# Kernel optimization log

Measured on AMD Instinct MI355X. Metric: run time of the kernel, lower is better.

## Reference

```python
import jax, jax.numpy as jnp
import numpy as np

K = 8          # opt.pk, explicit precision cutoff
MARGIN = 0.2   # opt.margin
NEG = -1e30    # sentinel for masked sort keys


def setup_inputs() -> dict:
    key = jax.random.key(0)
    k1, k2 = jax.random.split(key)
    batch_reprs = jax.random.normal(k1, (4096, 512), dtype=jnp.float32)
    batch_labels = jax.random.randint(k2, (4096,), 0, 64)
    return {"batch_reprs": batch_reprs, "batch_labels": batch_labels}


def _forward(batch_reprs, batch_labels):
    B = batch_reprs.shape[0]
    dt = batch_reprs.dtype
    # cls_match_mat: 1 if same class
    match = (batch_labels[:, None] == batch_labels[None, :]).astype(dt)
    # pairwise euclidean distance (squared=False), safe sqrt at zero diagonal
    sq = jnp.sum(batch_reprs * batch_reprs, axis=1)
    res = jnp.maximum(sq[:, None] - 2.0 * (batch_reprs @ batch_reprs.T) + sq[None, :], 0.0)
    zero = res <= 0.0
    d = jnp.where(zero, 0.0, jnp.sqrt(jnp.where(zero, 1.0, res)))
    sim_hat = -d + (1.0 - match) * MARGIN  # use_margin=True path
    # rank via double argsort (descending similarity -> rank 1 = best)
    order = jnp.argsort(-sim_hat, axis=1)
    rank = jnp.argsort(order, axis=1).astype(dt) + 1.0
    pos_nums = jnp.sum(match, axis=1)
    ks = jnp.minimum(pos_nums, jnp.asarray(K + 1, dt))[:, None]  # k_mat per row
    w = 1.0 / jnp.log2(rank + 1.0) + 1.0  # DCG-style rank weight
    # false positives: not same class, within top-k_i
    fp_mask = (match < 1.0) & (rank <= ks)
    fp_nums = jnp.sum(fp_mask, axis=1)  # |N| per row
    # false negatives: same class, beyond top-k_i
    fn_mask = (match > 0.0) & (rank > ks)
    fp_term = jnp.sum(jnp.where(fp_mask, sim_hat * w, 0.0))
    # per-row variable-size topk over false negatives, vectorized:
    # mask non-FN entries to -inf, sort desc, keep first fp_nums[i] entries
    fn_key = jnp.where(fn_mask, sim_hat, NEG)
    fn_order = jnp.argsort(-fn_key, axis=1)
    sorted_sim = jnp.take_along_axis(sim_hat, fn_order, axis=1)
    sorted_w = jnp.take_along_axis(w, fn_order, axis=1)
    sorted_valid = jnp.take_along_axis(fn_mask, fn_order, axis=1)
    take = (jnp.arange(B)[None, :].astype(dt) < fp_nums[:, None]) & sorted_valid
    fn_term = jnp.sum(jnp.where(take, sorted_sim * sorted_w, 0.0))
    # rows with fp_num==0 contribute 0 to both terms, matching the host loop
    return fp_term - fn_term


def reference(batch_reprs, batch_labels):
    return _forward(batch_reprs, batch_labels)
```

## Files before the change

kernel.cpp:

```cpp
#include <hip/hip_runtime.h>
#include <math.h>

#define BB 4096
#define DD 512
#define KTOP 9
#define MARGIN_F 0.2f

typedef __attribute__((ext_vector_type(8))) short short8;
typedef __attribute__((ext_vector_type(4))) float f32x4;
typedef unsigned long long u64;

__device__ unsigned short g_Rhi[(size_t)BB * DD];
__device__ u64 g_cmask[64 * 64];

__device__ __forceinline__ unsigned short f2bf(float x) {
  unsigned u = __float_as_uint(x);
  u += 0x7fffu + ((u >> 16) & 1u);
  return (unsigned short)(u >> 16);
}

__device__ __forceinline__ void gload16(void* lds, const void* g) {
  __builtin_amdgcn_global_load_lds(
      (const __attribute__((address_space(1))) void*)g,
      (__attribute__((address_space(3))) void*)lds, 16, 0, 0);
}

__device__ __forceinline__ float ord16val(unsigned o16) {
  unsigned e = (o16 << 16) | 0x8000u;
  unsigned s = (e & 0x80000000u) ? (e ^ 0x80000000u) : ~e;
  return __uint_as_float(s);
}

__device__ __forceinline__ unsigned wavemax32_dpp(unsigned c) {
#define MSTEP(CTRL, RM)                                                        \
  {                                                                            \
    unsigned o = (unsigned)__builtin_amdgcn_update_dpp(0, (int)c, CTRL, RM, 0xf, false); \
    if (o > c) c = o;                                                          \
  }
  MSTEP(0xB1, 0xf) MSTEP(0x4E, 0xf) MSTEP(0x141, 0xf) MSTEP(0x140, 0xf)
  MSTEP(0x142, 0xa) MSTEP(0x143, 0xc)
#undef MSTEP
  return (unsigned)__builtin_amdgcn_readlane((int)c, 63);
}

__device__ __forceinline__ int wavesum_dpp(int c) {
#define SSTEP(CTRL, RM)                                                        \
  c += __builtin_amdgcn_update_dpp(0, c, CTRL, RM, 0xf, false);
  SSTEP(0xB1, 0xf) SSTEP(0x4E, 0xf) SSTEP(0x141, 0xf) SSTEP(0x140, 0xf)
  SSTEP(0x142, 0xa) SSTEP(0x143, 0xc)
#undef SSTEP
  return __builtin_amdgcn_readlane(c, 63);
}

__device__ __forceinline__ unsigned u4c(const uint4& f, int q) {
  return q == 0 ? f.x : q == 1 ? f.y : q == 2 ? f.z : f.w;
}

__global__ __launch_bounds__(64) void splitsq(const float* __restrict__ R,
                                              float* __restrict__ sq) {
  const int row = blockIdx.x, lane = threadIdx.x;
  const float4* r4 = (const float4*)(R + (size_t)row * DD);
  float4 a = r4[lane], b = r4[lane + 64];
  float xs[8] = {a.x, a.y, a.z, a.w, b.x, b.y, b.z, b.w};
  unsigned short hs[8];
  float s = 0.f;
  #pragma unroll
  for (int q = 0; q < 8; ++q) {
    float x = xs[q];
    s += x * x;
    hs[q] = f2bf(x);
  }
  const size_t base = (size_t)row * DD;
  *(ushort4*)&g_Rhi[base + lane * 4]       = *(ushort4*)&hs[0];
  *(ushort4*)&g_Rhi[base + 256 + lane * 4] = *(ushort4*)&hs[4];
  #pragma unroll
  for (int off = 32; off; off >>= 1) s += __shfl_down(s, off);
  if (lane == 0) sq[row] = s;
}

__global__ __launch_bounds__(64) void buildmask(const int* __restrict__ labels) {
  __shared__ int slab[BB];
  const int c = blockIdx.x, lane = threadIdx.x;
  for (int i = lane; i < BB / 4; i += 64) ((int4*)slab)[i] = ((const int4*)labels)[i];
  __syncthreads();
  u64 m = 0;
  #pragma unroll
  for (int e = 0; e < 64; ++e) {
    int j = 512 * (e >> 3) + 8 * lane + (e & 7);
    m |= (u64)(slab[j] == c) << e;
  }
  g_cmask[c * 64 + lane] = m;
}

__global__ __launch_bounds__(256) void simgemm_sq(const int* __restrict__ labels,
                                                  const float* __restrict__ sq,
                                                  unsigned short* __restrict__ simq) {
  const int x = blockIdx.x & 7;
  const int c = blockIdx.x >> 3;
  const int bj = 4 * x + (c >> 5);
  const int bi = c & 31;
  const int i0 = bi * 128, j0 = bj * 128;

  __shared__ __align__(16) unsigned char smembytes[35840];
  unsigned short (*kbuf)[2][4096] = (unsigned short (*)[2][4096])smembytes;

  const int tid = threadIdx.x;
  const int wid = tid >> 6, lane = tid & 63;
  const int wr = wid >> 1, wc = wid & 1;
  const int lrow = lane & 15, kblk = lane >> 4;

  f32x4 acc[4][4] = {};

  auto stage = [&](int buf, int k0) {
    const int sr = lane & 15;
    const int sc = (lane >> 4) * 8;
    #pragma unroll
    for (int i = 0; i < 2; ++i) {
      const int chunk = 2 * wid + i;
      const int r = chunk * 16 + sr;
      gload16(&kbuf[buf][0][chunk * 512], &g_Rhi[(size_t)(i0 + r) * DD + k0 + sc]);
      gload16(&kbuf[buf][1][chunk * 512], &g_Rhi[(size_t)(j0 + r) * DD + k0 + sc]);
    }
  };

  stage(0, 0);

  for (int step = 0; step < 16; ++step) {
    const int cur = step & 1;
    __syncthreads();
    if (step < 15) stage(cur ^ 1, (step + 1) * 32);

    short8 a[4], b[4];
    #pragma unroll
    for (int m = 0; m < 4; ++m)
      a[m] = *(const short8*)&kbuf[cur][0][(wr * 4 + m) * 512 + lane * 8];
    #pragma unroll
    for (int n = 0; n < 4; ++n)
      b[n] = *(const short8*)&kbuf[cur][1][(wc * 4 + n) * 512 + lane * 8];

    #pragma unroll
    for (int m = 0; m < 4; ++m) {
      #pragma unroll
      for (int n = 0; n < 4; ++n) {
        acc[m][n] = __builtin_amdgcn_mfma_f32_16x16x32_bf16(a[m], b[n], acc[m][n], 0, 0, 0);
      }
    }
  }

  __syncthreads();
  unsigned short (*T)[132] = (unsigned short (*)[132])smembytes;
  float* sqi = (float*)(smembytes + 33792);
  float* sqj = (float*)(smembytes + 34304);
  int* labi  = (int*)(smembytes + 34816);
  int* labj  = (int*)(smembytes + 35328);
  if (tid < 128) { sqi[tid] = sq[i0 + tid]; labi[tid] = labels[i0 + tid]; }
  else { int t2 = tid - 128; sqj[t2] = sq[j0 + t2]; labj[t2] = labels[j0 + t2]; }
  __syncthreads();

  #pragma unroll
  for (int m = 0; m < 4; ++m) {
    const int rbase = wr * 64 + m * 16 + kblk * 4;
    #pragma unroll
    for (int n = 0; n < 4; ++n) {
      const int ccol = wc * 64 + n * 16 + lrow;
      const float sqc = sqj[ccol];
      const int lc_ = labj[ccol];
      #pragma unroll
      for (int reg = 0; reg < 4; ++reg) {
        const int r = rbase + reg;
        float res = sqi[r] - 2.0f * acc[m][n][reg] + sqc;
        float dd = (res <= 0.f) ? 0.f : sqrtf(res);
        float sv = -dd + ((labi[r] != lc_) ? MARGIN_F : 0.f);
        unsigned su = __float_as_uint(sv);
        unsigned ord = su ^ ((unsigned)((int)su >> 31) | 0x80000000u);
        T[r][ccol] = (unsigned short)(ord >> 16);
      }
    }
  }
  __syncthreads();

  const int srow0 = tid >> 4, scol0 = (tid & 15) * 8;
  #pragma unroll
  for (int p = 0; p < 8; ++p) {
    const int r = p * 16 + srow0;
    short8 w = *(const short8*)&T[r][scol0];
    *(short8*)&simq[(size_t)(i0 + r) * BB + j0 + scol0] = w;
  }
}

#define EKEY(e) ((((u4c(v[(e) >> 3], ((e) & 7) >> 1) >> (16 * ((e) & 1))) & 0xffffu) << 13) \
                 | (lbase - (unsigned)((512 * ((e) >> 3) + ((e) & 7)) << 1)                 \
                    + (unsigned)((mask >> (e)) & 1ull)))

#define TOP2UPD(k, a, b) {                                                     \
  unsigned _mx = ((k) > (a)) ? (k) : (a);                                      \
  unsigned _mn = ((k) > (a)) ? (a) : (k);                                      \
  (a) = _mx;                                                                   \
  (b) = (_mn > (b)) ? _mn : (b); }

__global__ __launch_bounds__(256) void rowproc6(const unsigned short* __restrict__ simq,
                                                const int* __restrict__ labels,
                                                float* __restrict__ partials) {
  const int tid = threadIdx.x;
  const int lane = tid & 63;
  const int row = blockIdx.x * 4 + (tid >> 6);

  const uint4* rowp = (const uint4*)(simq + (size_t)row * BB);
  uint4 v[8];
  #pragma unroll
  for (int s = 0; s < 8; ++s) v[s] = rowp[lane + s * 64];

  const int myl = labels[row];
  const u64 mask = g_cmask[myl * 64 + lane];
  const unsigned lbase = (unsigned)((4095 - 8 * lane) << 1);

  unsigned h1 = 0, h2 = 0;
  #pragma unroll
  for (int e = 0; e < 64; ++e) {
    unsigned k = EKEY(e);
    TOP2UPD(k, h1, h2);
  }
  const int pos = wavesum_dpp(__popcll(mask));
  const int ks = min(pos, KTOP);

  unsigned kth = 0;
  float fp = 0.f; int fpn = 0;
  #pragma unroll
  for (int t = 0; t < KTOP; ++t) {
    if (t < ks) {
      unsigned g = wavemax32_dpp(h1);
      if (!(g & 1u)) { fp += ord16val(g >> 13) * (1.f / log2f((float)(t + 2)) + 1.f); fpn++; }
      if (t == ks - 1) kth = g;
      if (h1 == g) {
        h1 = h2; h2 = ~0u;
        if (h1 == ~0u) {
          h1 = 0; h2 = 0;
          #pragma unroll
          for (int e = 0; e < 64; ++e) {
            unsigned k = EKEY(e);
            if (k < g) TOP2UPD(k, h1, h2);
          }
        }
      }
    }
  }

  float fn = 0.f;
  if (fpn > 0) {
    unsigned f1 = 0, f2 = 0;
    #pragma unroll
    for (int e = 0; e < 64; ++e) {
      unsigned k = EKEY(e);
      if ((k & 1u) && k < kth) TOP2UPD(k, f1, f2);
    }
    unsigned ck[KTOP];
    int nc = 0;
    #pragma unroll
    for (int u = 0; u < KTOP; ++u) {
      ck[u] = ~0u;
      if (u < fpn) {
        unsigned g = wavemax32_dpp(f1);
        if (g != 0u) {
          ck[u] = g; nc = u + 1;
          if (f1 == g) {
            f1 = f2; f2 = ~0u;
            if (f1 == ~0u) {
              f1 = 0; f2 = 0;
              #pragma unroll
              for (int e = 0; e < 64; ++e) {
                unsigned k = EKEY(e);
                if ((k & 1u) && k < g) TOP2UPD(k, f1, f2);
              }
            }
          }
        }
      }
    }
    if (nc > 0) {
      int cnt[KTOP];
      #pragma unroll
      for (int u = 0; u < KTOP; ++u) cnt[u] = 0;
      #pragma unroll
      for (int e = 0; e < 64; ++e) {
        unsigned k = EKEY(e);
        #pragma unroll
        for (int u = 0; u < KTOP; ++u) cnt[u] += (k > ck[u]) ? 1 : 0;
      }
      #pragma unroll
      for (int u = 0; u < KTOP; ++u) cnt[u] = wavesum_dpp(cnt[u]);
      #pragma unroll
      for (int u = 0; u < KTOP; ++u) {
        if (u < nc) {
          int rank = 1 + cnt[u];
          fn += ord16val(ck[u] >> 13) * (1.f / log2f((float)(rank + 1)) + 1.f);
        }
      }
    }
  }

  if (lane == 0) partials[row] = fp - fn;
}

__global__ __launch_bounds__(256) void finalreduce(const float* __restrict__ partials,
                                                   float* __restrict__ out) {
  __shared__ float s[256];
  const int tid = threadIdx.x;
  float acc = 0.f;
  for (int j = tid; j < BB; j += 256) acc += partials[j];
  s[tid] = acc; __syncthreads();
  #pragma unroll
  for (int st = 128; st; st >>= 1) { if (tid < st) s[tid] += s[tid + st]; __syncthreads(); }
  if (tid == 0) out[0] = s[0];
}

extern "C" void kernel_launch(void* const* d_in, const int* in_sizes, int n_in,
                              void* d_out, int out_size, void* d_ws, size_t ws_size,
                              hipStream_t stream) {
  const float* R      = (const float*)d_in[0];
  const int*   labels = (const int*)d_in[1];
  float* out = (float*)d_out;

  unsigned short* simq = (unsigned short*)d_ws;
  float* sq            = (float*)((char*)d_ws + (size_t)BB * BB * 2);
  float* partials      = sq + BB;

  splitsq<<<BB, 64, 0, stream>>>(R, sq);
  buildmask<<<64, 64, 0, stream>>>(labels);
  simgemm_sq<<<1024, 256, 0, stream>>>(labels, sq, simq);
  rowproc6<<<BB / 4, 256, 0, stream>>>(simq, labels, partials);
  finalreduce<<<1, 256, 0, stream>>>(partials, out);
}
```

Baseline: 101.7 us.

## Load GEMM operand fragments directly from global memory into registers

```diff
diff --git a/kernel.cpp b/kernel.cpp
--- a/kernel.cpp
+++ b/kernel.cpp
@@ -17,12 +17,6 @@
   unsigned u = __float_as_uint(x);
   u += 0x7fffu + ((u >> 16) & 1u);
   return (unsigned short)(u >> 16);
-}
-
-__device__ __forceinline__ void gload16(void* lds, const void* g) {
-  __builtin_amdgcn_global_load_lds(
-      (const __attribute__((address_space(1))) void*)g,
-      (__attribute__((address_space(3))) void*)lds, 16, 0, 0);
 }
 
 __device__ __forceinline__ float ord16val(unsigned o16) {
@@ -92,9 +86,9 @@
   g_cmask[c * 64 + lane] = m;
 }
 
-__global__ __launch_bounds__(256) void simgemm_sq(const int* __restrict__ labels,
-                                                  const float* __restrict__ sq,
-                                                  unsigned short* __restrict__ simq) {
+__global__ __launch_bounds__(256) void simgemm_reg(const int* __restrict__ labels,
+                                                   const float* __restrict__ sq,
+                                                   unsigned short* __restrict__ simq) {
   const int x = blockIdx.x & 7;
   const int c = blockIdx.x >> 3;
   const int bj = 4 * x + (c >> 5);
@@ -102,52 +96,49 @@
   const int i0 = bi * 128, j0 = bj * 128;
 
   __shared__ __align__(16) unsigned char smembytes[35840];
-  unsigned short (*kbuf)[2][4096] = (unsigned short (*)[2][4096])smembytes;
 
   const int tid = threadIdx.x;
   const int wid = tid >> 6, lane = tid & 63;
   const int wr = wid >> 1, wc = wid & 1;
   const int lrow = lane & 15, kblk = lane >> 4;
 
+  const unsigned short* pA[4];
+  const unsigned short* pB[4];
+  #pragma unroll
+  for (int m = 0; m < 4; ++m) {
+    pA[m] = g_Rhi + (size_t)(i0 + wr * 64 + m * 16 + lrow) * DD + kblk * 8;
+    pB[m] = g_Rhi + (size_t)(j0 + wc * 64 + m * 16 + lrow) * DD + kblk * 8;
+  }
+
   f32x4 acc[4][4] = {};
-
-  auto stage = [&](int buf, int k0) {
-    const int sr = lane & 15;
-    const int sc = (lane >> 4) * 8;
-    #pragma unroll
-    for (int i = 0; i < 2; ++i) {
-      const int chunk = 2 * wid + i;
-      const int r = chunk * 16 + sr;
-      gload16(&kbuf[buf][0][chunk * 512], &g_Rhi[(size_t)(i0 + r) * DD + k0 + sc]);
-      gload16(&kbuf[buf][1][chunk * 512], &g_Rhi[(size_t)(j0 + r) * DD + k0 + sc]);
-    }
-  };
-
-  stage(0, 0);
-
+  short8 fa[2][4], fb[2][4];
+
+  #pragma unroll
+  for (int m = 0; m < 4; ++m) {
+    fa[0][m] = *(const short8*)(pA[m]);
+    fb[0][m] = *(const short8*)(pB[m]);
+  }
+
+  #pragma unroll
   for (int step = 0; step < 16; ++step) {
     const int cur = step & 1;
-    __syncthreads();
-    if (step < 15) stage(cur ^ 1, (step + 1) * 32);
-
-    short8 a[4], b[4];
-    #pragma unroll
-    for (int m = 0; m < 4; ++m)
-      a[m] = *(const short8*)&kbuf[cur][0][(wr * 4 + m) * 512 + lane * 8];
-    #pragma unroll
-    for (int n = 0; n < 4; ++n)
-      b[n] = *(const short8*)&kbuf[cur][1][(wc * 4 + n) * 512 + lane * 8];
-
+    if (step < 15) {
+      const int koff = (step + 1) * 32;
+      #pragma unroll
+      for (int m = 0; m < 4; ++m) {
+        fa[cur ^ 1][m] = *(const short8*)(pA[m] + koff);
+        fb[cur ^ 1][m] = *(const short8*)(pB[m] + koff);
+      }
+    }
     #pragma unroll
     for (int m = 0; m < 4; ++m) {
       #pragma unroll
       for (int n = 0; n < 4; ++n) {
-        acc[m][n] = __builtin_amdgcn_mfma_f32_16x16x32_bf16(a[m], b[n], acc[m][n], 0, 0, 0);
-      }
-    }
-  }
-
-  __syncthreads();
+        acc[m][n] = __builtin_amdgcn_mfma_f32_16x16x32_bf16(fa[cur][m], fb[cur][n], acc[m][n], 0, 0, 0);
+      }
+    }
+  }
+
   unsigned short (*T)[132] = (unsigned short (*)[132])smembytes;
   float* sqi = (float*)(smembytes + 33792);
   float* sqj = (float*)(smembytes + 34304);
@@ -326,7 +317,7 @@
 
   splitsq<<<BB, 64, 0, stream>>>(R, sq);
   buildmask<<<64, 64, 0, stream>>>(labels);
-  simgemm_sq<<<1024, 256, 0, stream>>>(labels, sq, simq);
+  simgemm_reg<<<1024, 256, 0, stream>>>(labels, sq, simq);
   rowproc6<<<BB / 4, 256, 0, stream>>>(simq, labels, partials);
   finalreduce<<<1, 256, 0, stream>>>(partials, out);
 }
```

Measured after the change: 123.7 us. 1.22x slower.
